# Performance work log

Hardware: AMD Instinct MI355X
Metric: run time of the kernel (lower is better)

## Reference

```python
import jax, jax.numpy as jnp
import numpy as np

B = 256
SOM = (64, 64)
LAT = 64


def setup_inputs() -> dict:
    key = jax.random.key(0)
    ks = jax.random.split(key, 20)
    rn = lambda k, s: jax.random.normal(k, s, dtype=jnp.float32)
    W = 0.1  # small weight scale so exp(0.5*logvar) stays tame
    return {
        "x": rn(ks[0], (B, 1)),
        "eps": rn(ks[1], (B, LAT)),
        "embeddings": rn(ks[2], (SOM[0], SOM[1], LAT)),
        "w_e0": rn(ks[3], (1, 10)) * W, "b_e0": rn(ks[4], (10,)) * W,
        "w_e1": rn(ks[5], (10, 50)) * W, "b_e1": rn(ks[6], (50,)) * W,
        "w_mu": rn(ks[7], (50, LAT)) * W, "b_mu": rn(ks[8], (LAT,)) * W,
        "w_lv": rn(ks[9], (50, LAT)) * W, "b_lv": rn(ks[10], (LAT,)) * W,
        "w_d": rn(ks[11], (LAT, 100)) * W, "b_d": rn(ks[12], (100,)) * W,
        "w_d0": rn(ks[13], (100, 60)) * W, "b_d0": rn(ks[14], (60,)) * W,
        "w_d1": rn(ks[15], (60, 30)) * W, "b_d1": rn(ks[16], (30,)) * W,
        "w_d2": rn(ks[17], (30, 1)) * W, "b_d2": rn(ks[18], (1,)) * W,
    }


def _lrelu(v):
    return jax.nn.leaky_relu(v, 0.01)  # torch LeakyReLU default slope


def reference(x, eps, embeddings, w_e0, b_e0, w_e1, b_e1, w_mu, b_mu,
              w_lv, b_lv, w_d, b_d, w_d0, b_d0, w_d1, b_d1, w_d2, b_d2):
    # ---- encode ----
    h = _lrelu(x @ w_e0 + b_e0)
    h = _lrelu(h @ w_e1 + b_e1)
    mu = h @ w_mu + b_mu
    logvar = h @ w_lv + b_lv
    # ---- reparameterize ----
    z_e = mu + eps * jnp.exp(0.5 * logvar)                      # [B, L]
    # ---- get_z_q: full pairwise sq-distance to SOM grid ----
    s0, s1, _ = embeddings.shape
    diff = embeddings[None, :, :, :] - z_e[:, None, None, :]    # [B, S0, S1, L]
    z_dist = jnp.sum(diff * diff, axis=-1)                      # [B, S0, S1]
    n_min = jnp.argmin(z_dist.reshape(z_e.shape[0], -1), axis=-1)
    n_x = n_min // s1
    n_y = n_min % s1
    z_q = embeddings[n_x, n_y]                                  # [B, L]
    # ---- neighbors (faithful to original, incl. z_q_right bug) ----
    x_not_top = n_x < s0 - 1
    x_not_bottom = n_x > 0
    y_not_left = n_y > 0
    x_up = jnp.where(x_not_top, n_x + 1, n_x)
    x_down = jnp.where(x_not_bottom, n_x - 1, n_x)
    y_left = jnp.where(y_not_left, n_y - 1, n_y)
    z_q_up = jnp.where(x_not_top[:, None], embeddings[x_up, n_y], 0.0)
    z_q_down = jnp.where(x_not_bottom[:, None], embeddings[x_down, n_y], 0.0)
    # original code uses `==` instead of `=` for the right neighbor -> stays zero
    z_q_right = jnp.zeros_like(z_q)
    z_q_left = jnp.where(y_not_left[:, None], embeddings[n_x, y_left], 0.0)
    z_q_neighbors = jnp.stack([z_q, z_q_up, z_q_down, z_q_right, z_q_left], axis=1)
    # ---- decode (note: LeakyReLU on the final layer too, as in original) ----
    def decode(z):
        t = _lrelu(z @ w_d + b_d)
        t = _lrelu(t @ w_d0 + b_d0)
        t = _lrelu(t @ w_d1 + b_d1)
        return _lrelu(t @ w_d2 + b_d2)
    decoder_q = decode(z_q)
    decoder_e = decode(z_e)
    return (z_e, z_q, z_q_neighbors, decoder_e, decoder_q)
```

## Files before the change

### kernel.cpp

```cpp
#include <hip/hip_runtime.h>

__device__ __forceinline__ float lrelu(float v) { return v >= 0.f ? v : 0.01f * v; }

__device__ __forceinline__ unsigned long long shfl_down_u64(unsigned long long v, int off, int width) {
    unsigned lo = (unsigned)(v & 0xffffffffu);
    unsigned hi = (unsigned)(v >> 32);
    lo = __shfl_down(lo, off, width);
    hi = __shfl_down(hi, off, width);
    return ((unsigned long long)hi << 32) | lo;
}
__device__ __forceinline__ unsigned long long u64min(unsigned long long a, unsigned long long b) {
    return a < b ? a : b;
}

__device__ __forceinline__ float dist16(float4 r0, float4 r1, float4 r2, float4 r3,
                                        float4 z0, float4 z1, float4 z2, float4 z3) {
    float p = 0.f, d;
    d = r0.x - z0.x; p = fmaf(d, d, p);
    d = r0.y - z0.y; p = fmaf(d, d, p);
    d = r0.z - z0.z; p = fmaf(d, d, p);
    d = r0.w - z0.w; p = fmaf(d, d, p);
    d = r1.x - z1.x; p = fmaf(d, d, p);
    d = r1.y - z1.y; p = fmaf(d, d, p);
    d = r1.z - z1.z; p = fmaf(d, d, p);
    d = r1.w - z1.w; p = fmaf(d, d, p);
    d = r2.x - z2.x; p = fmaf(d, d, p);
    d = r2.y - z2.y; p = fmaf(d, d, p);
    d = r2.z - z2.z; p = fmaf(d, d, p);
    d = r2.w - z2.w; p = fmaf(d, d, p);
    d = r3.x - z3.x; p = fmaf(d, d, p);
    d = r3.y - z3.y; p = fmaf(d, d, p);
    d = r3.z - z3.z; p = fmaf(d, d, p);
    d = r3.w - z3.w; p = fmaf(d, d, p);
    return p;
}

__global__ __launch_bounds__(1024) void vae_mega(
    const float* __restrict__ x, const float* __restrict__ eps,
    const float* __restrict__ emb,
    const float* __restrict__ w_e0, const float* __restrict__ b_e0,
    const float* __restrict__ w_e1, const float* __restrict__ b_e1,
    const float* __restrict__ w_mu, const float* __restrict__ b_mu,
    const float* __restrict__ w_lv, const float* __restrict__ b_lv,
    const float* __restrict__ w_d,  const float* __restrict__ b_d,
    const float* __restrict__ w_d0, const float* __restrict__ b_d0,
    const float* __restrict__ w_d1, const float* __restrict__ b_d1,
    const float* __restrict__ w_d2, const float* __restrict__ b_d2,
    float* __restrict__ out,
    unsigned long long* __restrict__ wsK,
    unsigned int* __restrict__ wsC)
{
    const int bt   = blockIdx.x >> 2;
    const int rt   = blockIdx.x & 3;
    const int tid  = threadIdx.x;
    const int w    = tid >> 6;
    const int lane = tid & 63;

    __shared__ __align__(16) float L_wmu[3200], L_wlv[3200], L_we1[500];
    __shared__ float L_we0[10], L_be0[10], L_be1[50], L_bmu[64], L_blv[64];
    __shared__ __align__(16) float L_wd[6400], L_wd0[6000], L_wd1[1800];
    __shared__ float L_bd[100], L_bd0[60], L_bd1[30], L_wd2[30];

    __shared__ float h1s[4][52];
    __shared__ __align__(16) float zs[4][64];
    __shared__ __align__(16) float zq_s[4][64];
    __shared__ unsigned long long cand[4][16];
    __shared__ int nmin_s[4];
    __shared__ int fin_s;
    __shared__ float t0s[4][2][100];
    __shared__ float t1s[4][2][60];
    __shared__ float t2s[4][2][30];

    {
        const float4* s4; float4* d4;
        s4 = (const float4*)w_mu; d4 = (float4*)L_wmu;
        for (int i = tid; i < 800; i += 1024) d4[i] = s4[i];
        s4 = (const float4*)w_lv; d4 = (float4*)L_wlv;
        for (int i = tid; i < 800; i += 1024) d4[i] = s4[i];
        s4 = (const float4*)w_e1; d4 = (float4*)L_we1;
        for (int i = tid; i < 125; i += 1024) d4[i] = s4[i];
        if (tid < 10) { L_we0[tid] = w_e0[tid]; L_be0[tid] = b_e0[tid]; }
        if (tid < 50) L_be1[tid] = b_e1[tid];
        if (tid < 64) { L_bmu[tid] = b_mu[tid]; L_blv[tid] = b_lv[tid]; }
    }
    __syncthreads();

    if (w < 4) {
        const int j = bt * 4 + w;
        if (lane < 50) {
            const float xv = x[j];
            float acc = L_be1[lane];
            #pragma unroll
            for (int i = 0; i < 10; ++i) {
                float h = lrelu(fmaf(xv, L_we0[i], L_be0[i]));
                acc = fmaf(h, L_we1[i * 50 + lane], acc);
            }
            h1s[w][lane] = lrelu(acc);
        }
        float mu = L_bmu[lane];
        float lv = L_blv[lane];
        for (int i = 0; i < 50; ++i) {
            float h = h1s[w][i];
            mu = fmaf(h, L_wmu[i * 64 + lane], mu);
            lv = fmaf(h, L_wlv[i * 64 + lane], lv);
        }
        zs[w][lane] = fmaf(eps[j * 64 + lane], expf(0.5f * lv), mu);
    }
    __syncthreads();

    const int g = lane >> 2;
    const int q = lane & 3;
    const int rowBase = rt * 1024 + w * 64 + g;

    float4 zr[4][4];
    #pragma unroll
    for (int t = 0; t < 4; ++t) {
        const float* zb = &zs[t][q * 16];
        zr[t][0] = *reinterpret_cast<const float4*>(zb + 0);
        zr[t][1] = *reinterpret_cast<const float4*>(zb + 4);
        zr[t][2] = *reinterpret_cast<const float4*>(zb + 8);
        zr[t][3] = *reinterpret_cast<const float4*>(zb + 12);
    }
    unsigned long long bestT[4] = {~0ull, ~0ull, ~0ull, ~0ull};
    #pragma unroll
    for (int k = 0; k < 4; ++k) {
        const float* rp = emb + (rowBase + k * 16) * 64 + q * 16;
        const float4 r0 = *reinterpret_cast<const float4*>(rp + 0);
        const float4 r1 = *reinterpret_cast<const float4*>(rp + 4);
        const float4 r2 = *reinterpret_cast<const float4*>(rp + 8);
        const float4 r3 = *reinterpret_cast<const float4*>(rp + 12);
        #pragma unroll
        for (int t = 0; t < 4; ++t) {
            float p = dist16(r0, r1, r2, r3, zr[t][0], zr[t][1], zr[t][2], zr[t][3]);
            p += __shfl_xor(p, 1);
            p += __shfl_xor(p, 2);
            const unsigned long long key =
                ((unsigned long long)__float_as_uint(p) << 32) |
                (unsigned)(rowBase + k * 16);
            bestT[t] = u64min(bestT[t], key);
        }
    }
    #pragma unroll
    for (int t = 0; t < 4; ++t) {
        unsigned long long best = bestT[t];
        #pragma unroll
        for (int off = 32; off >= 4; off >>= 1)
            best = u64min(best, shfl_down_u64(best, off, 64));
        if (lane == 0) cand[t][w] = best;
    }
    __syncthreads();

    if (tid < 64) {
        const int t = tid >> 4, s = tid & 15;
        unsigned long long k = cand[t][s];
        #pragma unroll
        for (int off = 8; off > 0; off >>= 1)
            k = u64min(k, shfl_down_u64(k, off, 16));
        if (s == 0)
            atomicExch(&wsK[(bt * 4 + rt) * 8 + t], k);
        if (tid == 0) {
            __threadfence();
            const unsigned old = atomicAdd(&wsC[bt * 16], 1u);
            fin_s = ((old & 3u) == 3u);
        }
    }
    __syncthreads();
    if (!fin_s) return;

    if (tid < 16) {
        unsigned long long k =
            atomicOr(&wsK[(bt * 4 + (tid >> 2)) * 8 + (tid & 3)], 0ull);
        k = u64min(k, shfl_down_u64(k, 8, 16));
        k = u64min(k, shfl_down_u64(k, 4, 16));
        if (tid < 4) nmin_s[tid] = (int)(k & 0xffffffffu);
    }
    {
        const float4* s4; float4* d4;
        s4 = (const float4*)w_d;  d4 = (float4*)L_wd;
        for (int i = tid; i < 1600; i += 1024) d4[i] = s4[i];
        s4 = (const float4*)w_d0; d4 = (float4*)L_wd0;
        for (int i = tid; i < 1500; i += 1024) d4[i] = s4[i];
        s4 = (const float4*)w_d1; d4 = (float4*)L_wd1;
        for (int i = tid; i < 450; i += 1024) d4[i] = s4[i];
        if (tid < 100) L_bd[tid]  = b_d[tid];
        if (tid < 60)  L_bd0[tid] = b_d0[tid];
        if (tid < 30)  { L_bd1[tid] = b_d1[tid]; L_wd2[tid] = w_d2[tid]; }
    }
    __syncthreads();

    if (w >= 8 && w < 12) {
        const int i = w - 8;
        const int b = bt * 4 + i;
        const int nmin = nmin_s[i];
        const int nx = nmin >> 6, ny = nmin & 63;
        const int j = lane;
        out[b * 64 + j] = zs[i][j];
        const float zq = emb[nmin * 64 + j];
        zq_s[i][j] = zq;
        out[16384 + b * 64 + j] = zq;
        const int nb = 32768 + b * 320;
        out[nb + j] = zq;
        float up = (nx < 63) ? emb[((nx + 1) * 64 + ny) * 64 + j] : 0.f;
        out[nb + 64 + j] = up;
        float dn = (nx > 0) ? emb[((nx - 1) * 64 + ny) * 64 + j] : 0.f;
        out[nb + 128 + j] = dn;
        out[nb + 192 + j] = 0.f;
        float lf = (ny > 0) ? emb[(nx * 64 + (ny - 1)) * 64 + j] : 0.f;
        out[nb + 256 + j] = lf;
    }
    __syncthreads();

    const int di  = w >> 1;
    const int sel = w & 1;
    const bool dec = (w < 8);
    const float* zv = sel ? zq_s[di] : zs[di];

    if (dec) {
        for (int jj = lane; jj < 100; jj += 64) {
            float acc = L_bd[jj];
            for (int i = 0; i < 64; ++i)
                acc = fmaf(zv[i], L_wd[i * 100 + jj], acc);
            t0s[di][sel][jj] = lrelu(acc);
        }
    }
    __syncthreads();
    if (dec && lane < 60) {
        float acc = L_bd0[lane];
        for (int i = 0; i < 100; ++i)
            acc = fmaf(t0s[di][sel][i], L_wd0[i * 60 + lane], acc);
        t1s[di][sel][lane] = lrelu(acc);
    }
    __syncthreads();
    if (dec && lane < 30) {
        float acc = L_bd1[lane];
        for (int i = 0; i < 60; ++i)
            acc = fmaf(t1s[di][sel][i], L_wd1[i * 30 + lane], acc);
        t2s[di][sel][lane] = lrelu(acc);
    }
    __syncthreads();
    if (dec && lane == 0) {
        float acc = b_d2[0];
        for (int i = 0; i < 30; ++i)
            acc = fmaf(t2s[di][sel][i], L_wd2[i], acc);
        const float r = lrelu(acc);
        out[(sel ? 114944 : 114688) + bt * 4 + di] = r;
    }
}

extern "C" void kernel_launch(void* const* d_in, const int* in_sizes, int n_in,
                              void* d_out, int out_size, void* d_ws, size_t ws_size,
                              hipStream_t stream) {
    (void)in_sizes; (void)n_in; (void)ws_size; (void)out_size;
    const float* x    = (const float*)d_in[0];
    const float* eps  = (const float*)d_in[1];
    const float* emb  = (const float*)d_in[2];
    const float* w_e0 = (const float*)d_in[3];
    const float* b_e0 = (const float*)d_in[4];
    const float* w_e1 = (const float*)d_in[5];
    const float* b_e1 = (const float*)d_in[6];
    const float* w_mu = (const float*)d_in[7];
    const float* b_mu = (const float*)d_in[8];
    const float* w_lv = (const float*)d_in[9];
    const float* b_lv = (const float*)d_in[10];
    const float* w_d  = (const float*)d_in[11];
    const float* b_d  = (const float*)d_in[12];
    const float* w_d0 = (const float*)d_in[13];
    const float* b_d0 = (const float*)d_in[14];
    const float* w_d1 = (const float*)d_in[15];
    const float* b_d1 = (const float*)d_in[16];
    const float* w_d2 = (const float*)d_in[17];
    const float* b_d2 = (const float*)d_in[18];
    float* out = (float*)d_out;
    unsigned long long* wsK = (unsigned long long*)d_ws;
    unsigned int* wsC = (unsigned int*)((char*)d_ws + 65536);

    vae_mega<<<256, 1024, 0, stream>>>(
        x, eps, emb, w_e0, b_e0, w_e1, b_e1, w_mu, b_mu, w_lv, b_lv,
        w_d, b_d, w_d0, b_d0, w_d1, b_d1, w_d2, b_d2, out, wsK, wsC);
}
```

Before: 23.28 us.

## Prefetch embedding rows and decoder weights early to overlap with encoder

Each thread now loads the first two of its four embedding rows into registers before the encoder runs, pinned with empty asm so the loads are issued early, which hides their global-memory latency behind the encoder MLP. The decoder weight and bias copies into shared memory move from the last-finishing block's tail to the kernel prologue, so every block does them but off the critical path. The z_e output write moves into the encoder, done by rt==0 blocks, and several small loops get unroll pragmas. The cost is higher register pressure and redundant decoder-weight traffic in blocks that exit early.

```diff
diff --git a/kernel.cpp b/kernel.cpp
--- a/kernel.cpp
+++ b/kernel.cpp
@@ -35,6 +35,8 @@
     return p;
 }
 
+#define PIN4(v) asm volatile("" : "+v"(v.x), "+v"(v.y), "+v"(v.z), "+v"(v.w))
+
 __global__ __launch_bounds__(1024) void vae_mega(
     const float* __restrict__ x, const float* __restrict__ eps,
     const float* __restrict__ emb,
@@ -71,6 +73,22 @@
     __shared__ float t1s[4][2][60];
     __shared__ float t2s[4][2][30];
 
+    const int g = lane >> 2;
+    const int q = lane & 3;
+    const int rowBase = rt * 1024 + w * 64 + g;
+    const float* rp0 = emb + (rowBase +  0) * 64 + q * 16;
+    const float* rp1 = emb + (rowBase + 16) * 64 + q * 16;
+    float4 ea0 = *reinterpret_cast<const float4*>(rp0 + 0);
+    float4 ea1 = *reinterpret_cast<const float4*>(rp0 + 4);
+    float4 ea2 = *reinterpret_cast<const float4*>(rp0 + 8);
+    float4 ea3 = *reinterpret_cast<const float4*>(rp0 + 12);
+    float4 eb0 = *reinterpret_cast<const float4*>(rp1 + 0);
+    float4 eb1 = *reinterpret_cast<const float4*>(rp1 + 4);
+    float4 eb2 = *reinterpret_cast<const float4*>(rp1 + 8);
+    float4 eb3 = *reinterpret_cast<const float4*>(rp1 + 12);
+    PIN4(ea0); PIN4(ea1); PIN4(ea2); PIN4(ea3);
+    PIN4(eb0); PIN4(eb1); PIN4(eb2); PIN4(eb3);
+
     {
         const float4* s4; float4* d4;
         s4 = (const float4*)w_mu; d4 = (float4*)L_wmu;
@@ -79,9 +97,18 @@
         for (int i = tid; i < 800; i += 1024) d4[i] = s4[i];
         s4 = (const float4*)w_e1; d4 = (float4*)L_we1;
         for (int i = tid; i < 125; i += 1024) d4[i] = s4[i];
+        s4 = (const float4*)w_d;  d4 = (float4*)L_wd;
+        for (int i = tid; i < 1600; i += 1024) d4[i] = s4[i];
+        s4 = (const float4*)w_d0; d4 = (float4*)L_wd0;
+        for (int i = tid; i < 1500; i += 1024) d4[i] = s4[i];
+        s4 = (const float4*)w_d1; d4 = (float4*)L_wd1;
+        for (int i = tid; i < 450; i += 1024) d4[i] = s4[i];
         if (tid < 10) { L_we0[tid] = w_e0[tid]; L_be0[tid] = b_e0[tid]; }
         if (tid < 50) L_be1[tid] = b_e1[tid];
         if (tid < 64) { L_bmu[tid] = b_mu[tid]; L_blv[tid] = b_lv[tid]; }
+        if (tid < 100) L_bd[tid]  = b_d[tid];
+        if (tid < 60)  L_bd0[tid] = b_d0[tid];
+        if (tid < 30)  { L_bd1[tid] = b_d1[tid]; L_wd2[tid] = w_d2[tid]; }
     }
     __syncthreads();
 
@@ -99,18 +126,19 @@
         }
         float mu = L_bmu[lane];
         float lv = L_blv[lane];
+        #pragma unroll
         for (int i = 0; i < 50; ++i) {
             float h = h1s[w][i];
             mu = fmaf(h, L_wmu[i * 64 + lane], mu);
             lv = fmaf(h, L_wlv[i * 64 + lane], lv);
         }
-        zs[w][lane] = fmaf(eps[j * 64 + lane], expf(0.5f * lv), mu);
-    }
-    __syncthreads();
-
-    const int g = lane >> 2;
-    const int q = lane & 3;
-    const int rowBase = rt * 1024 + w * 64 + g;
+        const float z = fmaf(eps[j * 64 + lane], expf(0.5f * lv), mu);
+        zs[w][lane] = z;
+        if (rt == 0) out[j * 64 + lane] = z;
+    }
+    __syncthreads();
+    PIN4(ea0); PIN4(ea1); PIN4(ea2); PIN4(ea3);
+    PIN4(eb0); PIN4(eb1); PIN4(eb2); PIN4(eb3);
 
     float4 zr[4][4];
     #pragma unroll
@@ -124,11 +152,16 @@
     unsigned long long bestT[4] = {~0ull, ~0ull, ~0ull, ~0ull};
     #pragma unroll
     for (int k = 0; k < 4; ++k) {
-        const float* rp = emb + (rowBase + k * 16) * 64 + q * 16;
-        const float4 r0 = *reinterpret_cast<const float4*>(rp + 0);
-        const float4 r1 = *reinterpret_cast<const float4*>(rp + 4);
-        const float4 r2 = *reinterpret_cast<const float4*>(rp + 8);
-        const float4 r3 = *reinterpret_cast<const float4*>(rp + 12);
+        float4 r0, r1, r2, r3;
+        if (k == 0)      { r0 = ea0; r1 = ea1; r2 = ea2; r3 = ea3; }
+        else if (k == 1) { r0 = eb0; r1 = eb1; r2 = eb2; r3 = eb3; }
+        else {
+            const float* rp = emb + (rowBase + k * 16) * 64 + q * 16;
+            r0 = *reinterpret_cast<const float4*>(rp + 0);
+            r1 = *reinterpret_cast<const float4*>(rp + 4);
+            r2 = *reinterpret_cast<const float4*>(rp + 8);
+            r3 = *reinterpret_cast<const float4*>(rp + 12);
+        }
         #pragma unroll
         for (int t = 0; t < 4; ++t) {
             float p = dist16(r0, r1, r2, r3, zr[t][0], zr[t][1], zr[t][2], zr[t][3]);
@@ -174,18 +207,6 @@
         k = u64min(k, shfl_down_u64(k, 4, 16));
         if (tid < 4) nmin_s[tid] = (int)(k & 0xffffffffu);
     }
-    {
-        const float4* s4; float4* d4;
-        s4 = (const float4*)w_d;  d4 = (float4*)L_wd;
-        for (int i = tid; i < 1600; i += 1024) d4[i] = s4[i];
-        s4 = (const float4*)w_d0; d4 = (float4*)L_wd0;
-        for (int i = tid; i < 1500; i += 1024) d4[i] = s4[i];
-        s4 = (const float4*)w_d1; d4 = (float4*)L_wd1;
-        for (int i = tid; i < 450; i += 1024) d4[i] = s4[i];
-        if (tid < 100) L_bd[tid]  = b_d[tid];
-        if (tid < 60)  L_bd0[tid] = b_d0[tid];
-        if (tid < 30)  { L_bd1[tid] = b_d1[tid]; L_wd2[tid] = w_d2[tid]; }
-    }
     __syncthreads();
 
     if (w >= 8 && w < 12) {
@@ -194,7 +215,6 @@
         const int nmin = nmin_s[i];
         const int nx = nmin >> 6, ny = nmin & 63;
         const int j = lane;
-        out[b * 64 + j] = zs[i][j];
         const float zq = emb[nmin * 64 + j];
         zq_s[i][j] = zq;
         out[16384 + b * 64 + j] = zq;
@@ -218,6 +238,7 @@
     if (dec) {
         for (int jj = lane; jj < 100; jj += 64) {
             float acc = L_bd[jj];
+            #pragma unroll 16
             for (int i = 0; i < 64; ++i)
                 acc = fmaf(zv[i], L_wd[i * 100 + jj], acc);
             t0s[di][sel][jj] = lrelu(acc);
@@ -226,6 +247,7 @@
     __syncthreads();
     if (dec && lane < 60) {
         float acc = L_bd0[lane];
+        #pragma unroll 10
         for (int i = 0; i < 100; ++i)
             acc = fmaf(t0s[di][sel][i], L_wd0[i * 60 + lane], acc);
         t1s[di][sel][lane] = lrelu(acc);
@@ -233,6 +255,7 @@
     __syncthreads();
     if (dec && lane < 30) {
         float acc = L_bd1[lane];
+        #pragma unroll 10
         for (int i = 0; i < 60; ++i)
             acc = fmaf(t1s[di][sel][i], L_wd1[i * 30 + lane], acc);
         t2s[di][sel][lane] = lrelu(acc);
@@ -240,6 +263,7 @@
     __syncthreads();
     if (dec && lane == 0) {
         float acc = b_d2[0];
+        #pragma unroll
         for (int i = 0; i < 30; ++i)
             acc = fmaf(t2s[di][sel][i], L_wd2[i], acc);
         const float r = lrelu(acc);
```

Measured after the change: 24.45 us. +5.0%, slower.
